# Optimization experiments

Hardware: AMD Instinct MI355X
Metric: run time of the kernel (lower is better)

## Reference

```python
import jax, jax.numpy as jnp
import numpy as np

GRID = 24          # sqrt(576)
MM = 1024          # mm_hidden_size
HID = 4096         # hidden_size
HEADS = 8          # mm_hidden_size // 128
NQ = GRID * GRID   # 576 queries / tokens
BATCH = 16
K = 2              # top-k == num_experts == 2


def _sincos_1d(d, pos):
    omega = np.arange(d // 2, dtype=np.float32) / (d / 2.0)
    omega = 1.0 / 10000 ** omega
    out = np.einsum('m,d->md', pos.reshape(-1).astype(np.float32), omega)
    return np.concatenate([np.sin(out), np.cos(out)], axis=1)


def _sincos_2d(d, g):
    gw, gh = np.meshgrid(np.arange(g, dtype=np.float32), np.arange(g, dtype=np.float32))
    return np.concatenate([_sincos_1d(d // 2, gh), _sincos_1d(d // 2, gw)], axis=1)


def layer_norm(x, g, b, eps=1e-5):
    mu = x.mean(-1, keepdims=True)
    var = ((x - mu) ** 2).mean(-1, keepdims=True)
    return (x - mu) * jax.lax.rsqrt(var + eps) * g + b


def mha(q, k, v, Wi, bi, Wo, bo, H):
    # q,k,v: [N, S, D]; Wi: [3D, D]; torch nn.MultiheadAttention semantics
    N, S, D = q.shape
    dh = D // H
    Wq, Wk, Wv = Wi[:D], Wi[D:2 * D], Wi[2 * D:]
    bq, bk, bv = bi[:D], bi[D:2 * D], bi[2 * D:]
    qp = (q @ Wq.T + bq).reshape(N, S, H, dh)
    kp = (k @ Wk.T + bk).reshape(N, -1, H, dh)
    vp = (v @ Wv.T + bv).reshape(N, -1, H, dh)
    scale = jnp.asarray(1.0 / np.sqrt(dh), q.dtype)
    scores = jnp.einsum('bqhd,bkhd->bhqk', qp, kp) * scale
    attn = jax.nn.softmax(scores, axis=-1)
    out = jnp.einsum('bhqk,bkhd->bqhd', attn, vp).reshape(N, S, D)
    return out @ Wo.T + bo


def _gating(xf, w_gate, w_noise, noise):
    # noisy top-k gating, training mode, k == num_experts == 2
    clean = xf @ w_gate                               # [B, 2]
    std = jax.nn.softplus(xf @ w_noise) + 0.01
    logits = jax.nn.softmax(clean + noise * std, axis=1)
    top_vals, top_idx = jax.lax.top_k(logits, K)      # min(k+1, n) == 2
    gates_k = top_vals / (top_vals.sum(1, keepdims=True) + 1e-6)
    rows = jnp.arange(xf.shape[0])[:, None]
    return jnp.zeros_like(logits).at[rows, top_idx].set(gates_k)


def setup_inputs() -> dict:
    key = jax.random.key(0)
    ks = jax.random.split(key, 10)
    s = 0.02
    f32 = jnp.float32
    return dict(
        x=jax.random.normal(ks[0], (BATCH, NQ, MM), f32),
        noise=jax.random.normal(ks[1], (BATCH * NQ, 2), f32),
        W1=jax.random.normal(ks[2], (HID, MM), f32) * s,
        b1=jnp.zeros((HID,), f32),
        W2=jax.random.normal(ks[3], (HID, HID), f32) * s,
        b2=jnp.zeros((HID,), f32),
        query=jax.random.normal(ks[4], (NQ, MM), f32) * s,
        pos_embed=jnp.asarray(_sincos_2d(MM, GRID), f32),
        ln_q_g=jnp.ones((MM,), f32), ln_q_b=jnp.zeros((MM,), f32),
        ln_kv_g=jnp.ones((MM,), f32), ln_kv_b=jnp.zeros((MM,), f32),
        in_proj_w=jax.random.normal(ks[5], (3 * MM, MM), f32) * s,
        in_proj_b=jnp.zeros((3 * MM,), f32),
        out_w=jax.random.normal(ks[6], (MM, MM), f32) * s,
        out_b=jnp.zeros((MM,), f32),
        w_gate=jax.random.normal(ks[7], (MM, 2), f32) * s,
        w_noise=jax.random.normal(ks[8], (MM, 2), f32) * s,
    )


def reference(x, noise, W1, b1, W2, b2, query, pos_embed, ln_q_g, ln_q_b,
              ln_kv_g, ln_kv_b, in_proj_w, in_proj_b, out_w, out_b,
              w_gate, w_noise):
    N, C, D = x.shape

    def projection(t):  # Linear -> GELU(exact) -> Linear
        h = jax.nn.gelu(t @ W1.T + b1, approximate=False)
        return h @ W2.T + b2

    # --- Resampler expert (kv_proj/ln_post/proj are identity here) ---
    kv = layer_norm(x, ln_kv_g, ln_kv_b)                    # [N, 576, D]
    q = layer_norm(query, ln_q_g, ln_q_b) + pos_embed       # [576, D]
    q = jnp.broadcast_to(q, (N, C, D))
    attn_out = mha(q, kv + pos_embed, kv, in_proj_w, in_proj_b, out_w, out_b, HEADS)

    e0 = projection(x)          # expert 0: MLP projection
    e1 = projection(attn_out)   # expert 1: resampler then projection

    gates = _gating(x.reshape(N * C, D), w_gate, w_noise, noise).reshape(N, C, 2)
    # stack(...,-1) @ gates[...,None] squeezed == gated sum over experts
    return e0 * gates[..., 0:1] + e1 * gates[..., 1:2]
```

## Files before the change

kernel.cpp:

```cpp
#include <hip/hip_runtime.h>
#include <hip/hip_bf16.h>
#include <cstdint>
#include <cstddef>


typedef __bf16 bf16;
typedef __bf16 bf16x4 __attribute__((ext_vector_type(4)));
typedef __bf16 bf16x8 __attribute__((ext_vector_type(8)));
typedef float  f32x4  __attribute__((ext_vector_type(4)));

#define BATCH 16
#define NQ    576
#define MM    1024
#define HID   4096
#define HEADS 8
#define DH    128
#define ROWS  (BATCH*NQ)

typedef const unsigned int __attribute__((address_space(1)))* gas_ptr;
typedef unsigned int __attribute__((address_space(3)))* las_ptr;

__device__ __forceinline__ void async16(const bf16* g, bf16* l) {
  __builtin_amdgcn_global_load_lds((gas_ptr)g, (las_ptr)l, 16, 0, 0);
}

__global__ __launch_bounds__(256) void cvt_kernel(
    const float* __restrict__ s, bf16* __restrict__ d)
{
  const int i = (blockIdx.x * 256 + threadIdx.x) * 4;
  f32x4 v = *(const f32x4*)(s + i);
  bf16x4 o;
#pragma unroll
  for (int j = 0; j < 4; ++j) o[j] = (bf16)v[j];
  *(bf16x4*)(d + i) = o;
}

enum { MODE_BIAS = 0, MODE_GG = 1, MODE_GGACC = 2, MODE_GB = 3 };

template <int MODE, typename OutT>
__global__ __launch_bounds__(256) void gemm_bt(
    const bf16* __restrict__ A, const bf16* __restrict__ W,
    const float* __restrict__ bias, OutT* __restrict__ C,
    const float* __restrict__ gates, int M, int N, int K)
{
  __shared__ bf16 As[128 * 64];
  __shared__ bf16 Bs[128 * 64];

  const int tid  = threadIdx.x;
  const int lane = tid & 63;
  const int w    = tid >> 6;
  const int wm   = (w & 1) * 64;
  const int wn   = (w >> 1) * 64;
  const int l15  = lane & 15;
  const int quad = lane >> 4;
  const int m0   = blockIdx.y * 128;
  const int n0   = blockIdx.x * 128;

  f32x4 acc[4][4] = {};

  const int srow0  = tid >> 3;
  const int schunk = (tid & 7) ^ (srow0 & 7);
  int arows[4], brows[4];
#pragma unroll
  for (int j = 0; j < 4; ++j) {
    int r = m0 + j * 32 + srow0; if (r > M - 1) r = M - 1;
    arows[j] = r;
    brows[j] = n0 + j * 32 + srow0;
  }
  const int kc = schunk * 8;
  bf16* lA = As + tid * 8;
  bf16* lB = Bs + tid * 8;

  const int axb  = (quad ^ (l15 & 7)) * 8;
  const int axb1 = axb ^ 32;

  for (int kt = 0; kt < K; kt += 64) {
#pragma unroll
    for (int j = 0; j < 4; ++j)
      async16(A + (size_t)arows[j] * K + kt + kc, lA + j * 2048);
#pragma unroll
    for (int j = 0; j < 4; ++j)
      async16(W + (size_t)brows[j] * K + kt + kc, lB + j * 2048);
    __syncthreads();

    bf16x8 af[4], bfr[4];
#pragma unroll
    for (int i = 0; i < 4; ++i)
      af[i] = *(const bf16x8*)(As + (wm + i * 16 + l15) * 64 + axb);
#pragma unroll
    for (int i = 0; i < 4; ++i)
      bfr[i] = *(const bf16x8*)(Bs + (wn + i * 16 + l15) * 64 + axb);
#pragma unroll
    for (int mi = 0; mi < 4; ++mi)
#pragma unroll
      for (int ni = 0; ni < 4; ++ni)
        acc[mi][ni] = __builtin_amdgcn_mfma_f32_16x16x32_bf16(
            af[mi], bfr[ni], acc[mi][ni], 0, 0, 0);
#pragma unroll
    for (int i = 0; i < 4; ++i)
      af[i] = *(const bf16x8*)(As + (wm + i * 16 + l15) * 64 + axb1);
#pragma unroll
    for (int i = 0; i < 4; ++i)
      bfr[i] = *(const bf16x8*)(Bs + (wn + i * 16 + l15) * 64 + axb1);
#pragma unroll
    for (int mi = 0; mi < 4; ++mi)
#pragma unroll
      for (int ni = 0; ni < 4; ++ni)
        acc[mi][ni] = __builtin_amdgcn_mfma_f32_16x16x32_bf16(
            af[mi], bfr[ni], acc[mi][ni], 0, 0, 0);
    __syncthreads();
  }

#pragma unroll
  for (int ni = 0; ni < 4; ++ni) {
    const int col = n0 + wn + ni * 16 + l15;
    const float bv = bias[col];
#pragma unroll
    for (int mi = 0; mi < 4; ++mi) {
      const int rowb = m0 + wm + mi * 16 + quad * 4;
#pragma unroll
      for (int r = 0; r < 4; ++r) {
        const int gr = rowb + r;
        if (gr < M) {
          const size_t idx = (size_t)gr * N + col;
          if (MODE == MODE_GB) {
            C[idx] = (OutT)(acc[mi][ni][r] +
                            (gates[gr * 2] + gates[gr * 2 + 1]) * bv);
          } else {
            float v = acc[mi][ni][r] + bv;
            if (MODE == MODE_GG || MODE == MODE_GGACC)
              v = 0.5f * v * (1.0f + erff(v * 0.70710678118654752f));
            if (MODE == MODE_GG)
              C[idx] = (OutT)(v * gates[gr * 2]);
            else if (MODE == MODE_GGACC)
              C[idx] = (OutT)((float)C[idx] + v * gates[gr * 2 + 1]);
            else
              C[idx] = (OutT)v;
          }
        }
      }
    }
  }
}

__global__ __launch_bounds__(256) void attn_kernel(
    const bf16* __restrict__ qp, const bf16* __restrict__ kp,
    const bf16* __restrict__ vp, bf16* __restrict__ ctx)
{
  __shared__ bf16 Qs[64 * 128];
  __shared__ bf16 Ks[64 * 128];
  __shared__ bf16 Vt[128 * 64];
  __shared__ bf16 Ps[64 * 64];

  const int qt = blockIdx.x, b = blockIdx.y, h = blockIdx.z;
  const int tid = threadIdx.x, lane = tid & 63, w = tid >> 6;
  const int l15 = lane & 15, quad = lane >> 4;
  const int q0 = qt * 64;
  const int sw = l15 & 7;

#pragma unroll
  for (int i = 0; i < 4; ++i) {
    const int c = i * 256 + tid;
    const int row = c >> 4, ch = c & 15;
    *(bf16x8*)(Qs + row * 128 + ((ch ^ (row & 7)) << 3)) =
        *(const bf16x8*)(qp + (size_t)(q0 + row) * MM + h * DH + ch * 8);
  }

  float m_r[4], l_r[4];
  f32x4 accO[8] = {};
#pragma unroll
  for (int r = 0; r < 4; ++r) { m_r[r] = -1e30f; l_r[r] = 0.f; }

  const float scale = 0.08838834764831843f;

  for (int kt = 0; kt < 9; ++kt) {
    __syncthreads();
    const int kbase = b * NQ + kt * 64;
#pragma unroll
    for (int i = 0; i < 4; ++i) {
      const int c = i * 256 + tid;
      const int row = c >> 4, ch = c & 15;
      *(bf16x8*)(Ks + row * 128 + ((ch ^ (row & 7)) << 3)) =
          *(const bf16x8*)(kp + (size_t)(kbase + row) * MM + h * DH + ch * 8);
      bf16x8 vv = *(const bf16x8*)(vp + (size_t)(kbase + row) * MM + h * DH + ch * 8);
#pragma unroll
      for (int j = 0; j < 8; ++j) Vt[(ch * 8 + j) * 64 + row] = vv[j];
    }
    __syncthreads();

    f32x4 sacc[4] = {};
#pragma unroll
    for (int kcq = 0; kcq < 4; ++kcq) {
      bf16x8 aq = *(const bf16x8*)(Qs + (w * 16 + l15) * 128 +
                                   (((kcq * 4 + quad) ^ sw) << 3));
#pragma unroll
      for (int ni = 0; ni < 4; ++ni) {
        bf16x8 bk = *(const bf16x8*)(Ks + (ni * 16 + l15) * 128 +
                                     (((kcq * 4 + quad) ^ sw) << 3));
        sacc[ni] = __builtin_amdgcn_mfma_f32_16x16x32_bf16(aq, bk, sacc[ni], 0, 0, 0);
      }
    }
#pragma unroll
    for (int ni = 0; ni < 4; ++ni)
#pragma unroll
      for (int r = 0; r < 4; ++r) sacc[ni][r] *= scale;

    float p[4][4];
#pragma unroll
    for (int r = 0; r < 4; ++r) {
      float mx = fmaxf(fmaxf(sacc[0][r], sacc[1][r]), fmaxf(sacc[2][r], sacc[3][r]));
#pragma unroll
      for (int off = 8; off >= 1; off >>= 1) mx = fmaxf(mx, __shfl_xor(mx, off, 64));
      const float mnew = fmaxf(m_r[r], mx);
      const float al = expf(m_r[r] - mnew);
      float rs = 0.f;
#pragma unroll
      for (int ni = 0; ni < 4; ++ni) { p[ni][r] = expf(sacc[ni][r] - mnew); rs += p[ni][r]; }
#pragma unroll
      for (int off = 8; off >= 1; off >>= 1) rs += __shfl_xor(rs, off, 64);
      l_r[r] = l_r[r] * al + rs;
      m_r[r] = mnew;
#pragma unroll
      for (int ni2 = 0; ni2 < 8; ++ni2) accO[ni2][r] *= al;
    }

#pragma unroll
    for (int ni = 0; ni < 4; ++ni)
#pragma unroll
      for (int r = 0; r < 4; ++r) {
        const int prow = w * 16 + quad * 4 + r;
        const int k = ni * 16 + l15;
        Ps[prow * 64 + (((k >> 3) ^ (prow & 7)) << 3) + (k & 7)] = (bf16)p[ni][r];
      }

#pragma unroll
    for (int kc2 = 0; kc2 < 2; ++kc2) {
      bf16x8 ap = *(const bf16x8*)(Ps + (w * 16 + l15) * 64 +
                                   (((kc2 * 4 + quad) ^ sw) << 3));
#pragma unroll
      for (int ni2 = 0; ni2 < 8; ++ni2) {
        bf16x8 bv = *(const bf16x8*)(Vt + (ni2 * 16 + l15) * 64 + kc2 * 32 + quad * 8);
        accO[ni2] = __builtin_amdgcn_mfma_f32_16x16x32_bf16(ap, bv, accO[ni2], 0, 0, 0);
      }
    }
  }

#pragma unroll
  for (int r = 0; r < 4; ++r) {
    const float inv = 1.0f / l_r[r];
    const int qrow = q0 + w * 16 + quad * 4 + r;
#pragma unroll
    for (int ni2 = 0; ni2 < 8; ++ni2)
      ctx[(size_t)(b * NQ + qrow) * MM + h * DH + ni2 * 16 + l15] =
          (bf16)(accO[ni2][r] * inv);
  }
}

__global__ __launch_bounds__(256) void lnx_kernel(
    const float* __restrict__ x, const float* __restrict__ g,
    const float* __restrict__ bta, const float* __restrict__ pos,
    const float* __restrict__ wg, const float* __restrict__ wn,
    const float* __restrict__ noise,
    bf16* __restrict__ kv, bf16* __restrict__ kin,
    bf16* __restrict__ x_bf, float* __restrict__ gates)
{
  const int row = blockIdx.x, tid = threadIdx.x;
  f32x4 xv = *(const f32x4*)(x + (size_t)row * MM + tid * 4);

  float s = 0.f, ss = 0.f, a0 = 0.f, a1 = 0.f, c0 = 0.f, c1 = 0.f;
#pragma unroll
  for (int j = 0; j < 4; ++j) {
    const int c = tid * 4 + j;
    s  += xv[j];
    ss += xv[j] * xv[j];
    a0 += xv[j] * wg[c * 2];
    a1 += xv[j] * wg[c * 2 + 1];
    c0 += xv[j] * wn[c * 2];
    c1 += xv[j] * wn[c * 2 + 1];
  }

  {
    bf16x4 o;
#pragma unroll
    for (int j = 0; j < 4; ++j) o[j] = (bf16)xv[j];
    *(bf16x4*)(x_bf + (size_t)row * MM + tid * 4) = o;
  }

#pragma unroll
  for (int off = 32; off >= 1; off >>= 1) {
    s  += __shfl_xor(s,  off, 64);  ss += __shfl_xor(ss, off, 64);
    a0 += __shfl_xor(a0, off, 64);  a1 += __shfl_xor(a1, off, 64);
    c0 += __shfl_xor(c0, off, 64);  c1 += __shfl_xor(c1, off, 64);
  }
  __shared__ float red[24];
  const int w = tid >> 6;
  if ((tid & 63) == 0) {
    red[w * 6]     = s;  red[w * 6 + 1] = ss;
    red[w * 6 + 2] = a0; red[w * 6 + 3] = a1;
    red[w * 6 + 4] = c0; red[w * 6 + 5] = c1;
  }
  __syncthreads();
  s  = red[0] + red[6]  + red[12] + red[18];
  ss = red[1] + red[7]  + red[13] + red[19];

  const float mu   = s * (1.0f / MM);
  const float rsig = rsqrtf(ss * (1.0f / MM) - mu * mu + 1e-5f);
  const int prow = row % NQ;
#pragma unroll
  for (int j = 0; j < 4; ++j) {
    const int c = tid * 4 + j;
    const float y = (xv[j] - mu) * rsig * g[c] + bta[c];
    kv[(size_t)row * MM + c]  = (bf16)y;
    kin[(size_t)row * MM + c] = (bf16)(y + pos[(size_t)prow * MM + c]);
  }

  if (tid == 0) {
    a0 = red[2] + red[8]  + red[14] + red[20];
    a1 = red[3] + red[9]  + red[15] + red[21];
    c0 = red[4] + red[10] + red[16] + red[22];
    c1 = red[5] + red[11] + red[17] + red[23];
    const float sp0 = fmaxf(c0, 0.f) + log1pf(expf(-fabsf(c0)));
    const float sp1 = fmaxf(c1, 0.f) + log1pf(expf(-fabsf(c1)));
    const float l0 = a0 + noise[row * 2]     * (sp0 + 0.01f);
    const float l1 = a1 + noise[row * 2 + 1] * (sp1 + 0.01f);
    const float mx = fmaxf(l0, l1);
    const float e0 = expf(l0 - mx), e1 = expf(l1 - mx);
    const float inv = 1.0f / (e0 + e1);
    const float p0 = e0 * inv, p1 = e1 * inv;
    const float den = 1.0f / (p0 + p1 + 1e-6f);
    gates[row * 2]     = p0 * den;
    gates[row * 2 + 1] = p1 * den;
  }
}

__global__ __launch_bounds__(256) void ln_q_kernel(
    const float* __restrict__ query, const float* __restrict__ g,
    const float* __restrict__ bta, const float* __restrict__ pos,
    bf16* __restrict__ qout)
{
  const int row = blockIdx.x, tid = threadIdx.x;
  f32x4 xv = *(const f32x4*)(query + (size_t)row * MM + tid * 4);
  float s = 0.f, ss = 0.f;
#pragma unroll
  for (int j = 0; j < 4; ++j) { s += xv[j]; ss += xv[j] * xv[j]; }
#pragma unroll
  for (int off = 32; off >= 1; off >>= 1) { s += __shfl_xor(s, off, 64); ss += __shfl_xor(ss, off, 64); }
  __shared__ float red[8];
  const int w = tid >> 6;
  if ((tid & 63) == 0) { red[w] = s; red[4 + w] = ss; }
  __syncthreads();
  s  = red[0] + red[1] + red[2] + red[3];
  ss = red[4] + red[5] + red[6] + red[7];
  const float mu = s * (1.0f / MM);
  const float rsig = rsqrtf(ss * (1.0f / MM) - mu * mu + 1e-5f);
#pragma unroll
  for (int j = 0; j < 4; ++j) {
    const int c = tid * 4 + j;
    const float y = (xv[j] - mu) * rsig * g[c] + bta[c] + pos[(size_t)row * MM + c];
    qout[(size_t)row * MM + c] = (bf16)y;
  }
}

extern "C" void kernel_launch(void* const* d_in, const int* in_sizes, int n_in,
                              void* d_out, int out_size, void* d_ws, size_t ws_size,
                              hipStream_t stream)
{
  const float* x       = (const float*)d_in[0];
  const float* noise   = (const float*)d_in[1];
  const float* W1      = (const float*)d_in[2];
  const float* b1      = (const float*)d_in[3];
  const float* W2      = (const float*)d_in[4];
  const float* b2      = (const float*)d_in[5];
  const float* query   = (const float*)d_in[6];
  const float* pos     = (const float*)d_in[7];
  const float* ln_q_g  = (const float*)d_in[8];
  const float* ln_q_b  = (const float*)d_in[9];
  const float* ln_kv_g = (const float*)d_in[10];
  const float* ln_kv_b = (const float*)d_in[11];
  const float* ipw     = (const float*)d_in[12];
  const float* ipb     = (const float*)d_in[13];
  const float* out_w   = (const float*)d_in[14];
  const float* out_b   = (const float*)d_in[15];
  const float* w_gate  = (const float*)d_in[16];
  const float* w_noise = (const float*)d_in[17];
  float* out = (float*)d_out;

  char* ws = (char*)d_ws;
  bf16*  kin   = (bf16*)(ws);
  bf16*  ctx   = kin;
  bf16*  kp    = (bf16*)(ws + 18874368);
  bf16*  vp    = (bf16*)(ws + 37748736);
  bf16*  qbuf  = (bf16*)(ws + 56623104);
  bf16*  qp    = (bf16*)(ws + 57802752);
  bf16*  ipwb  = (bf16*)(ws + 58982400);
  bf16*  outwb = (bf16*)(ws + 65273856);
  bf16*  h     = (bf16*)(ws);
  bf16*  x_bf  = (bf16*)(ws + 75497472);
  bf16*  W1b   = (bf16*)(ws + 94371840);
  bf16*  W2b   = (bf16*)(ws + 102760448);
  float* gates = (float*)(ws + 136314880);
  bf16*  kv       = (bf16*)d_out;
  bf16*  attn_out = (bf16*)((char*)d_out + 18874368);

  cvt_kernel<<<4096,  256, 0, stream>>>(W1, W1b);
  cvt_kernel<<<16384, 256, 0, stream>>>(W2, W2b);
  cvt_kernel<<<3072,  256, 0, stream>>>(ipw,   ipwb);
  cvt_kernel<<<1024,  256, 0, stream>>>(out_w, outwb);
  lnx_kernel<<<ROWS, 256, 0, stream>>>(x, ln_kv_g, ln_kv_b, pos,
                                       w_gate, w_noise, noise,
                                       kv, kin, x_bf, gates);
  ln_q_kernel<<<NQ, 256, 0, stream>>>(query, ln_q_g, ln_q_b, pos, qbuf);

  gemm_bt<MODE_BIAS, bf16><<<dim3(8, 5),  256, 0, stream>>>(qbuf, ipwb, ipb, qp, nullptr, NQ, MM, MM);
  gemm_bt<MODE_BIAS, bf16><<<dim3(8, 72), 256, 0, stream>>>(kin, ipwb + (size_t)MM * MM, ipb + MM, kp, nullptr, ROWS, MM, MM);
  gemm_bt<MODE_BIAS, bf16><<<dim3(8, 72), 256, 0, stream>>>(kv, ipwb + (size_t)2 * MM * MM, ipb + 2 * MM, vp, nullptr, ROWS, MM, MM);

  attn_kernel<<<dim3(9, BATCH, HEADS), 256, 0, stream>>>(qp, kp, vp, ctx);

  gemm_bt<MODE_BIAS, bf16><<<dim3(8, 72), 256, 0, stream>>>(ctx, outwb, out_b, attn_out, nullptr, ROWS, MM, MM);

  gemm_bt<MODE_GG,    bf16><<<dim3(32, 72), 256, 0, stream>>>(x_bf,     W1b, b1, h, gates, ROWS, HID, MM);
  gemm_bt<MODE_GGACC, bf16><<<dim3(32, 72), 256, 0, stream>>>(attn_out, W1b, b1, h, gates, ROWS, HID, MM);
  gemm_bt<MODE_GB,   float><<<dim3(32, 72), 256, 0, stream>>>(h,        W2b, b2, out, gates, ROWS, HID, HID);
}
```

Baseline: 1.373 ms.

## Pre-transpose V in separate kernel and use async LDS loads in attention

```diff
diff --git a/kernel.cpp b/kernel.cpp
--- a/kernel.cpp
+++ b/kernel.cpp
@@ -143,9 +143,40 @@
   }
 }
 
+__global__ __launch_bounds__(256) void vtr_kernel(
+    const bf16* __restrict__ vp, bf16* __restrict__ vT)
+{
+  __shared__ bf16 T[128 * 64];
+  const int kt = blockIdx.x, b = blockIdx.y, h = blockIdx.z;
+  const int tid = threadIdx.x;
+  const int k0 = kt * 64;
+
+#pragma unroll
+  for (int i = 0; i < 4; ++i) {
+    const int c = i * 256 + tid;
+    const int row = c >> 4, ch = c & 15;
+    bf16x8 v = *(const bf16x8*)(vp + (size_t)(b * NQ + k0 + row) * MM +
+                                h * DH + ch * 8);
+#pragma unroll
+    for (int j = 0; j < 8; ++j) {
+      const int d = ch * 8 + j;
+      T[d * 64 + (((row >> 3) ^ (d & 7)) << 3) + (row & 7)] = v[j];
+    }
+  }
+  __syncthreads();
+
+#pragma unroll
+  for (int i = 0; i < 4; ++i) {
+    const int c = i * 256 + tid;
+    const int drow = c >> 3, kch = c & 7;
+    bf16x8 v = *(const bf16x8*)(T + drow * 64 + ((kch ^ (drow & 7)) << 3));
+    *(bf16x8*)(vT + ((size_t)b * MM + h * DH + drow) * NQ + k0 + kch * 8) = v;
+  }
+}
+
 __global__ __launch_bounds__(256) void attn_kernel(
     const bf16* __restrict__ qp, const bf16* __restrict__ kp,
-    const bf16* __restrict__ vp, bf16* __restrict__ ctx)
+    const bf16* __restrict__ vT, bf16* __restrict__ ctx)
 {
   __shared__ bf16 Qs[64 * 128];
   __shared__ bf16 Ks[64 * 128];
@@ -162,8 +193,8 @@
   for (int i = 0; i < 4; ++i) {
     const int c = i * 256 + tid;
     const int row = c >> 4, ch = c & 15;
-    *(bf16x8*)(Qs + row * 128 + ((ch ^ (row & 7)) << 3)) =
-        *(const bf16x8*)(qp + (size_t)(q0 + row) * MM + h * DH + ch * 8);
+    async16(qp + (size_t)(q0 + row) * MM + h * DH + ((ch ^ (row & 7)) << 3),
+            Qs + c * 8);
   }
 
   float m_r[4], l_r[4];
@@ -172,19 +203,21 @@
   for (int r = 0; r < 4; ++r) { m_r[r] = -1e30f; l_r[r] = 0.f; }
 
   const float scale = 0.08838834764831843f;
+  const size_t vbase = ((size_t)b * MM + h * DH) * NQ;
 
   for (int kt = 0; kt < 9; ++kt) {
     __syncthreads();
     const int kbase = b * NQ + kt * 64;
+    const size_t vk = vbase + kt * 64;
 #pragma unroll
     for (int i = 0; i < 4; ++i) {
       const int c = i * 256 + tid;
       const int row = c >> 4, ch = c & 15;
-      *(bf16x8*)(Ks + row * 128 + ((ch ^ (row & 7)) << 3)) =
-          *(const bf16x8*)(kp + (size_t)(kbase + row) * MM + h * DH + ch * 8);
-      bf16x8 vv = *(const bf16x8*)(vp + (size_t)(kbase + row) * MM + h * DH + ch * 8);
-#pragma unroll
-      for (int j = 0; j < 8; ++j) Vt[(ch * 8 + j) * 64 + row] = vv[j];
+      async16(kp + (size_t)(kbase + row) * MM + h * DH + ((ch ^ (row & 7)) << 3),
+              Ks + c * 8);
+      const int drow = c >> 3, kch = c & 7;
+      async16(vT + vk + (size_t)drow * NQ + ((kch ^ (drow & 7)) << 3),
+              Vt + c * 8);
     }
     __syncthreads();
 
@@ -239,7 +272,8 @@
                                    (((kc2 * 4 + quad) ^ sw) << 3));
 #pragma unroll
       for (int ni2 = 0; ni2 < 8; ++ni2) {
-        bf16x8 bv = *(const bf16x8*)(Vt + (ni2 * 16 + l15) * 64 + kc2 * 32 + quad * 8);
+        bf16x8 bv = *(const bf16x8*)(Vt + (ni2 * 16 + l15) * 64 +
+                                     (((kc2 * 4 + quad) ^ sw) << 3));
         accO[ni2] = __builtin_amdgcn_mfma_f32_16x16x32_bf16(ap, bv, accO[ni2], 0, 0, 0);
       }
     }
@@ -400,6 +434,7 @@
   bf16*  W2b   = (bf16*)(ws + 102760448);
   float* gates = (float*)(ws + 136314880);
   bf16*  kv       = (bf16*)d_out;
+  bf16*  vT       = (bf16*)d_out;
   bf16*  attn_out = (bf16*)((char*)d_out + 18874368);
 
   cvt_kernel<<<4096,  256, 0, stream>>>(W1, W1b);
@@ -415,7 +450,8 @@
   gemm_bt<MODE_BIAS, bf16><<<dim3(8, 72), 256, 0, stream>>>(kin, ipwb + (size_t)MM * MM, ipb + MM, kp, nullptr, ROWS, MM, MM);
   gemm_bt<MODE_BIAS, bf16><<<dim3(8, 72), 256, 0, stream>>>(kv, ipwb + (size_t)2 * MM * MM, ipb + 2 * MM, vp, nullptr, ROWS, MM, MM);
 
-  attn_kernel<<<dim3(9, BATCH, HEADS), 256, 0, stream>>>(qp, kp, vp, ctx);
+  vtr_kernel<<<dim3(9, BATCH, HEADS), 256, 0, stream>>>(vp, vT);
+  attn_kernel<<<dim3(9, BATCH, HEADS), 256, 0, stream>>>(qp, kp, vT, ctx);
 
   gemm_bt<MODE_BIAS, bf16><<<dim3(8, 72), 256, 0, stream>>>(ctx, outwb, out_b, attn_out, nullptr, ROWS, MM, MM);
 
```

Result: faster. 1.237 ms (-9.9%).
